# Performance work log

Hardware: AMD Instinct MI355X
Metric: run time of the kernel (lower is better)

Reference implementation:

```python
import jax, jax.numpy as jnp
import numpy as np

BS, H, W, A, NC, G = 2048, 14, 14, 5, 2, 30
SIZE = 1 + NC + 4  # conf, classes, x, y, w, h
OBJ_SCALE, NOOBJ_SCALE, CLASS_SCALE, COORD_SCALE = 5.0, 0.5, 1.0, 1.0


def setup_inputs() -> dict:
    key = jax.random.key(0)
    pred = jax.random.normal(key, (BS, A * SIZE, H, W), dtype=jnp.float32) * 0.5
    # Structured label: G ground-truth boxes per image at distinct cells.
    rng = np.random.default_rng(0)
    lab = np.zeros((BS, 7, H, W), np.float32)
    perm = np.argsort(rng.random((BS, H * W)), axis=1)[:, :G]  # distinct cells
    r, c = perm // W, perm % W
    b = np.arange(BS)[:, None]
    lab[b, 0, r, c] = 1.0
    cls = rng.integers(0, 2, (BS, G)).astype(np.float32)
    lab[b, 1, r, c] = cls
    lab[b, 2, r, c] = 1.0 - cls
    lab[b, 3, r, c] = rng.uniform(0.1, 0.9, (BS, G))  # tx in-cell offset
    lab[b, 4, r, c] = rng.uniform(0.1, 0.9, (BS, G))  # ty
    lab[b, 5, r, c] = rng.uniform(0.05, 0.4, (BS, G))  # tw (normalized)
    lab[b, 6, r, c] = rng.uniform(0.05, 0.4, (BS, G))  # th
    anchors = np.array([[42.0, 44.0], [91.0, 104.0], [162.0, 220.0],
                        [299.0, 170.0], [396.0, 359.0]], np.float32)
    return {"pred": pred, "label": jnp.asarray(lab),
            "anchors": jnp.asarray(anchors), "seen": 6400}


def _yolo_v2_loss(pred, label, anchors, seen):
    f32 = jnp.float32
    anchor_bias = anchors / (512.0 / 14.0) / jnp.array([W, H], f32)  # [A,2], grid-normalized
    # [BS,H,W,A,SIZE]
    pred_r = pred.transpose(0, 2, 3, 1).reshape(BS, H, W, A, SIZE)
    sxy = jax.nn.sigmoid(pred_r[..., 1 + NC:3 + NC])               # sigmoid(x,y)
    ids = jnp.stack(jnp.meshgrid(jnp.arange(W, dtype=f32),
                                 jnp.arange(H, dtype=f32)), -1)[:, :, None, :]  # [H,W,1,2]=(c,r)
    coords = (sxy + ids) / jnp.array([W, H], f32)                  # normalized centers
    wh = jnp.exp(pred_r[..., 3 + NC:5 + NC]) * anchor_bias         # normalized w,h
    boxes = jnp.concatenate([coords, wh], -1)                      # [BS,H,W,A,4]
    aw, ah = anchor_bias[:, 0], anchor_bias[:, 1]

    def per_image(pred_b, sxy_b, boxes_b, label_b):
        obj = label_b[0].reshape(-1)
        vals, flat = jax.lax.top_k(obj, G)
        valid = vals > 0                                           # [G]
        r = flat // W
        c = flat % W
        tx, ty = label_b[3, r, c], label_b[4, r, c]
        tw = jnp.where(valid, label_b[5, r, c], 1.0)
        th = jnp.where(valid, label_b[6, r, c], 1.0)
        # gt boxes are built from detached .data in the torch code -> stop_gradient
        gx = jax.lax.stop_gradient((tx + c.astype(f32)) / W)
        gy = jax.lax.stop_gradient((ty + r.astype(f32)) / H)
        tw = jax.lax.stop_gradient(tw)
        th = jax.lax.stop_gradient(th)
        # pairwise IoU pred boxes [H,W,A] vs gt [G] -> [H,W,A,G]
        x1, y1 = boxes_b[..., 0:1], boxes_b[..., 1:2]
        w1, h1 = boxes_b[..., 2:3], boxes_b[..., 3:4]
        xi1 = jnp.maximum(x1 - 0.5 * w1, gx - 0.5 * tw)
        yi1 = jnp.maximum(y1 - 0.5 * h1, gy - 0.5 * th)
        xi2 = jnp.minimum(x1 + 0.5 * w1, gx + 0.5 * tw)
        yi2 = jnp.minimum(y1 + 0.5 * h1, gy + 0.5 * th)
        inter = jnp.maximum(xi2 - xi1, 0.0) * jnp.maximum(yi2 - yi1, 0.0)
        union = w1 * h1 + tw * th - inter
        iou = jnp.maximum(inter / union, 0.0)
        iou = jnp.where(valid, iou, 0.0)
        noobj = (iou.max(-1) <= 0.6).astype(f32) * (NOOBJ_SCALE * pred_b[..., 0])
        if seen < 12800:
            prior = 0.01 * jnp.concatenate([sxy_b - 0.5,
                                            pred_b[..., 3 + NC:5 + NC]], -1)
        else:
            prior = jnp.zeros((H, W, A, 4), f32)
        coord_obj = jnp.concatenate([prior, noobj[..., None]], -1)  # [H,W,A,5]
        # best anchor per gt (IoU of (0,0,tw,th) vs (0,0,aw,ah))
        ia = jnp.minimum(tw[:, None], aw) * jnp.minimum(th[:, None], ah)
        aid = jnp.argmax(ia / (tw[:, None] * th[:, None] + aw * ah - ia), axis=1)
        wi = (gx * W).astype(jnp.int32)
        fx = gx * W - wi.astype(f32)
        hj = (gy * H).astype(jnp.int32)
        fy = gy * H - hj.astype(f32)
        twh = jnp.log(jnp.stack([tw, th], 1) / anchor_bias[aid])    # [G,2]
        truth_coords = jnp.concatenate([fx[:, None], fy[:, None], twh], 1)
        p_sel = pred_b[hj, wi, aid]                                 # [G,SIZE]
        pc = jnp.concatenate([sxy_b[hj, wi, aid], p_sel[:, 3 + NC:5 + NC]], 1)
        wgt = COORD_SCALE * (2.0 - fx * fy)                         # detached in torch
        closs = wgt[:, None] * (pc - truth_coords)                  # [G,4]
        iou_sel = iou[hj, wi, aid, jnp.arange(G)]                   # [G]
        objl = OBJ_SCALE * (p_sel[:, 0] - iou_sel)
        tco = jnp.concatenate([closs, objl[:, None]], 1) * valid[:, None].astype(f32)
        cvec = jnp.stack([label_b[1, hj, wi], label_b[2, hj, wi]], 1)
        cls_l = CLASS_SCALE * (p_sel[:, 1:1 + NC] - cvec)
        loss_cls = jnp.sum((cls_l ** 2) * valid[:, None].astype(f32))
        m = jnp.zeros((H, W, A), f32).at[hj, wi, aid].add(valid.astype(f32))
        ta = jnp.zeros((H, W, A, 5), f32).at[hj, wi, aid].add(tco)
        m4 = m[..., None]
        comb = m4 * ta + (1.0 - m4) * coord_obj
        il = loss_cls + jnp.sum(comb ** 2)
        return jnp.where(jnp.any(valid), il, 0.0)

    losses = jax.vmap(per_image)(pred_r, sxy, boxes, label)
    return jnp.reshape(jnp.sum(losses) / BS, (1,))


def reference(pred, label, anchors, seen):
    return _yolo_v2_loss(pred, label, anchors, seen)
```

## Files before the change

kernel.cpp:

```cpp
#include <hip/hip_runtime.h>
#include <math.h>

#define BS 2048
#define H_ 14
#define W_ 14
#define A_ 5
#define G_ 30
#define HW_ 196
#define NCELL 980
#define NTHREADS 256
#define LABN (7 * HW_)
#define LAB4 (LABN / 4)

__device__ __forceinline__ float fast_rcp(float x) { return __builtin_amdgcn_rcpf(x); }

__global__ __launch_bounds__(NTHREADS) void yolo_main(
    const float* __restrict__ pred,
    const float* __restrict__ label,
    const float* __restrict__ anchors,
    float* __restrict__ partial)
{
    __shared__ float  s_lab[LABN];
    __shared__ float4 s_box[G_];
    __shared__ float  s_thr[G_];
    __shared__ float  s_area[G_];
    __shared__ float4 s_tgt[G_];
    __shared__ float4 s_aux[G_];
    __shared__ float  s_aw[A_], s_ah[A_];
    __shared__ short  s_map[NCELL];
    __shared__ int    s_flat[G_];
    __shared__ int    s_wcnt[NTHREADS / 64];
    __shared__ float  s_red[NTHREADS / 64];

    const int b    = blockIdx.x;
    const int tid  = threadIdx.x;
    const int lane = tid & 63;
    const int wv   = tid >> 6;
    const float* lb = label + (size_t)b * LABN;
    const float* pb = pred  + (size_t)b * (A_ * 7 * HW_);

    float objv = (tid < HW_) ? lb[tid] : 0.0f;

    {
        const float4* l4 = (const float4*)lb;
        float4* s4 = (float4*)s_lab;
        for (int i = tid; i < LAB4; i += NTHREADS) s4[i] = l4[i];
    }
    for (int i = tid; i < NCELL; i += NTHREADS) s_map[i] = -1;
    if (tid < A_) {
        const float div1 = 512.0f / 14.0f;
        s_aw[tid] = anchors[2 * tid]     / div1 / (float)W_;
        s_ah[tid] = anchors[2 * tid + 1] / div1 / (float)H_;
    }

    unsigned long long bm = __ballot(objv > 0.0f);
    if (lane == 0) s_wcnt[wv] = __popcll(bm);
    __syncthreads();
    if (objv > 0.0f) {
        int rank = __popcll(bm & ((1ULL << lane) - 1ULL));
        for (int w2 = 0; w2 < wv; ++w2) rank += s_wcnt[w2];
        s_flat[rank] = tid;
    }
    __syncthreads();

    if (tid < G_) {
        int flat = s_flat[tid];
        int r = flat / W_, c = flat - r * W_;
        float tx = s_lab[3 * HW_ + flat];
        float ty = s_lab[4 * HW_ + flat];
        float tw = s_lab[5 * HW_ + flat];
        float th = s_lab[6 * HW_ + flat];
        float gx = (tx + (float)c) / (float)W_;
        float gy = (ty + (float)r) / (float)H_;
        int   wi = (int)(gx * (float)W_);
        int   hj = (int)(gy * (float)H_);
        float fx = gx * (float)W_ - (float)wi;
        float fy = gy * (float)H_ - (float)hj;
        float best = -1.0f; int aid = 0;
        for (int aa = 0; aa < A_; ++aa) {
            float ia = fminf(tw, s_aw[aa]) * fminf(th, s_ah[aa]);
            float m  = ia / (tw * th + s_aw[aa] * s_ah[aa] - ia);
            if (m > best) { best = m; aid = aa; }
        }
        s_box[tid]  = make_float4(gx - 0.5f * tw, gy - 0.5f * th,
                                  gx + 0.5f * tw, gy + 0.5f * th);
        s_area[tid] = tw * th;
        s_thr[tid]  = 0.375f * tw * th;
        s_tgt[tid]  = make_float4(fx, fy, __logf(tw / s_aw[aid]), __logf(th / s_ah[aid]));
        s_aux[tid]  = make_float4(2.0f - fx * fy,
                                  s_lab[1 * HW_ + hj * W_ + wi],
                                  s_lab[2 * HW_ + hj * W_ + wi],
                                  0.0f);
        s_map[(hj * W_ + wi) * A_ + aid] = (short)tid;
    }
    __syncthreads();

    float lsum = 0.0f;
    if (tid < 245) {
        int a   = tid / 49;
        int q   = tid - a * 49;
        int hw0 = 4 * q;
        const float4* p4 = (const float4*)(pb + a * 7 * HW_);
        float4 P0 = p4[0 * 49 + q];
        float4 P1 = p4[1 * 49 + q];
        float4 P2 = p4[2 * 49 + q];
        float4 P3 = p4[3 * 49 + q];
        float4 P4 = p4[4 * 49 + q];
        float4 P5 = p4[5 * 49 + q];
        float4 P6 = p4[6 * 49 + q];
        float p0v[4] = {P0.x, P0.y, P0.z, P0.w};
        float p1v[4] = {P1.x, P1.y, P1.z, P1.w};
        float p2v[4] = {P2.x, P2.y, P2.z, P2.w};
        float p3v[4] = {P3.x, P3.y, P3.z, P3.w};
        float p4v[4] = {P4.x, P4.y, P4.z, P4.w};
        float p5v[4] = {P5.x, P5.y, P5.z, P5.w};
        float p6v[4] = {P6.x, P6.y, P6.z, P6.w};

        float aw = s_aw[a], ah = s_ah[a];
        float sxv[4], syv[4], xlo[4], xhi[4], ylo[4], yhi[4], acc[4];
        #pragma unroll
        for (int j = 0; j < 4; ++j) {
            int hw = hw0 + j;
            int h  = hw / W_;
            int w  = hw - h * W_;
            float sx = fast_rcp(1.0f + __expf(-p3v[j]));
            float sy = fast_rcp(1.0f + __expf(-p4v[j]));
            float bw = __expf(p5v[j]) * aw;
            float bh = __expf(p6v[j]) * ah;
            float x1 = (sx + (float)w) * (1.0f / (float)W_);
            float y1 = (sy + (float)h) * (1.0f / (float)H_);
            sxv[j] = sx;  syv[j] = sy;
            xlo[j] = x1 - 0.5f * bw;  xhi[j] = x1 + 0.5f * bw;
            ylo[j] = y1 - 0.5f * bh;  yhi[j] = y1 + 0.5f * bh;
            acc[j] = -1e30f;
        }

        #pragma unroll 5
        for (int g = 0; g < G_; ++g) {
            float4 bx  = s_box[g];
            float  thr = s_thr[g];
            #pragma unroll
            for (int j = 0; j < 4; ++j) {
                float xi1 = fmaxf(xlo[j], bx.x);
                float yi1 = fmaxf(ylo[j], bx.y);
                float xi2 = fminf(xhi[j], bx.z);
                float yi2 = fminf(yhi[j], bx.w);
                float dx = fmaxf(xi2 - xi1, 0.0f);
                float dy = fmaxf(yi2 - yi1, 0.0f);
                acc[j] = fmaxf(acc[j], fmaf(dx, dy, -thr));
            }
        }

        #pragma unroll
        for (int j = 0; j < 4; ++j) {
            int g_at = s_map[(hw0 + j) * A_ + a];
            float area1 = (xhi[j] - xlo[j]) * (yhi[j] - ylo[j]);
            if (g_at >= 0) {
                float4 t  = s_tgt[g_at];
                float4 u  = s_aux[g_at];
                float4 bx = s_box[g_at];
                float xi1 = fmaxf(xlo[j], bx.x);
                float yi1 = fmaxf(ylo[j], bx.y);
                float xi2 = fminf(xhi[j], bx.z);
                float yi2 = fminf(yhi[j], bx.w);
                float inter = fmaxf(xi2 - xi1, 0.0f) * fmaxf(yi2 - yi1, 0.0f);
                float uni   = area1 + s_area[g_at] - inter;
                float iou   = fmaxf(inter * fast_rcp(uni), 0.0f);
                float wg = u.x;
                float d0 = wg * (sxv[j] - t.x);
                float d1 = wg * (syv[j] - t.y);
                float d2 = wg * (p5v[j] - t.z);
                float d3 = wg * (p6v[j] - t.w);
                float ob = 5.0f * (p0v[j] - iou);
                float c1 = p1v[j] - u.y;
                float c2 = p2v[j] - u.z;
                lsum += d0*d0 + d1*d1 + d2*d2 + d3*d3 + ob*ob + c1*c1 + c2*c2;
            } else {
                float pr0 = 0.01f * (sxv[j] - 0.5f);
                float pr1 = 0.01f * (syv[j] - 0.5f);
                float pr2 = 0.01f * p5v[j];
                float pr3 = 0.01f * p6v[j];
                float no  = (acc[j] <= 0.375f * area1) ? 0.5f * p0v[j] : 0.0f;
                lsum += pr0*pr0 + pr1*pr1 + pr2*pr2 + pr3*pr3 + no*no;
            }
        }
    }

    #pragma unroll
    for (int off = 32; off > 0; off >>= 1)
        lsum += __shfl_down(lsum, off, 64);
    if (lane == 0) s_red[wv] = lsum;
    __syncthreads();
    if (tid == 0) {
        float tot = 0.0f;
        #pragma unroll
        for (int i = 0; i < NTHREADS / 64; ++i) tot += s_red[i];
        partial[b] = tot;
    }
}

__global__ __launch_bounds__(NTHREADS) void yolo_reduce(
    const float* __restrict__ partial, float* __restrict__ out)
{
    __shared__ float s_red[NTHREADS / 64];
    const int tid = threadIdx.x, lane = tid & 63, wv = tid >> 6;
    float s = 0.0f;
    for (int i = tid; i < BS; i += NTHREADS) s += partial[i];
    #pragma unroll
    for (int off = 32; off > 0; off >>= 1)
        s += __shfl_down(s, off, 64);
    if (lane == 0) s_red[wv] = s;
    __syncthreads();
    if (tid == 0) {
        float tot = 0.0f;
        #pragma unroll
        for (int i = 0; i < NTHREADS / 64; ++i) tot += s_red[i];
        out[0] = tot * (1.0f / (float)BS);
    }
}

extern "C" void kernel_launch(void* const* d_in, const int* in_sizes, int n_in,
                              void* d_out, int out_size, void* d_ws, size_t ws_size,
                              hipStream_t stream) {
    const float* pred    = (const float*)d_in[0];
    const float* label   = (const float*)d_in[1];
    const float* anchors = (const float*)d_in[2];
    float* out     = (float*)d_out;
    float* partial = (float*)d_ws;

    yolo_main<<<dim3(BS), dim3(NTHREADS), 0, stream>>>(pred, label, anchors, partial);
    yolo_reduce<<<dim3(1), dim3(NTHREADS), 0, stream>>>(partial, out);
}
```

Before: 115.1 us.

## Split each image across two single-wave blocks with two work items per lane

Each image is now handled by two 64-thread blocks instead of one 256-thread block. Each lane processes two anchor/quad work items, and the block reduction is a single wave shuffle with no shared-memory stage. The label load, gt-box extraction and target setup are now done redundantly by both blocks of an image, which doubles label reads and setup work, in exchange for lighter per-block synchronization and more, smaller blocks. The cell-to-gt map shrinks from short to char, and the reduce kernel sums twice as many partials.

```diff
diff --git a/kernel.cpp b/kernel.cpp
--- a/kernel.cpp
+++ b/kernel.cpp
@@ -7,14 +7,15 @@
 #define A_ 5
 #define G_ 30
 #define HW_ 196
-#define NCELL 980
-#define NTHREADS 256
 #define LABN (7 * HW_)
 #define LAB4 (LABN / 4)
+#define NTH 64
+#define NQ 245
+#define NBLK (BS * 2)
 
 __device__ __forceinline__ float fast_rcp(float x) { return __builtin_amdgcn_rcpf(x); }
 
-__global__ __launch_bounds__(NTHREADS) void yolo_main(
+__global__ __launch_bounds__(NTH, 4) void yolo_main(
     const float* __restrict__ pred,
     const float* __restrict__ label,
     const float* __restrict__ anchors,
@@ -27,44 +28,51 @@
     __shared__ float4 s_tgt[G_];
     __shared__ float4 s_aux[G_];
     __shared__ float  s_aw[A_], s_ah[A_];
-    __shared__ short  s_map[NCELL];
     __shared__ int    s_flat[G_];
-    __shared__ int    s_wcnt[NTHREADS / 64];
-    __shared__ float  s_red[NTHREADS / 64];
-
-    const int b    = blockIdx.x;
-    const int tid  = threadIdx.x;
-    const int lane = tid & 63;
-    const int wv   = tid >> 6;
+    __shared__ char   s_map[992] __attribute__((aligned(16)));
+
+    const int blk  = blockIdx.x;
+    const int b    = blk >> 1;
+    const int half = blk & 1;
+    const int lane = threadIdx.x;
     const float* lb = label + (size_t)b * LABN;
     const float* pb = pred  + (size_t)b * (A_ * 7 * HW_);
 
-    float objv = (tid < HW_) ? lb[tid] : 0.0f;
-
     {
         const float4* l4 = (const float4*)lb;
         float4* s4 = (float4*)s_lab;
-        for (int i = tid; i < LAB4; i += NTHREADS) s4[i] = l4[i];
-    }
-    for (int i = tid; i < NCELL; i += NTHREADS) s_map[i] = -1;
-    if (tid < A_) {
+        #pragma unroll
+        for (int k = 0; k < 6; ++k) {
+            int i = k * NTH + lane;
+            if (i < LAB4) s4[i] = l4[i];
+        }
+    }
+    if (lane < 62) ((int4*)s_map)[lane] = make_int4(-1, -1, -1, -1);
+    if (lane < A_) {
         const float div1 = 512.0f / 14.0f;
-        s_aw[tid] = anchors[2 * tid]     / div1 / (float)W_;
-        s_ah[tid] = anchors[2 * tid + 1] / div1 / (float)H_;
-    }
-
-    unsigned long long bm = __ballot(objv > 0.0f);
-    if (lane == 0) s_wcnt[wv] = __popcll(bm);
-    __syncthreads();
-    if (objv > 0.0f) {
-        int rank = __popcll(bm & ((1ULL << lane) - 1ULL));
-        for (int w2 = 0; w2 < wv; ++w2) rank += s_wcnt[w2];
-        s_flat[rank] = tid;
-    }
-    __syncthreads();
-
-    if (tid < G_) {
-        int flat = s_flat[tid];
+        s_aw[lane] = anchors[2 * lane]     / div1 / (float)W_;
+        s_ah[lane] = anchors[2 * lane + 1] / div1 / (float)H_;
+    }
+    __syncthreads();
+
+    {
+        int base = 0;
+        #pragma unroll
+        for (int k = 0; k < 4; ++k) {
+            int idx = k * NTH + lane;
+            float v = (idx < HW_) ? s_lab[idx] : 0.0f;
+            unsigned long long m = __ballot(v > 0.0f);
+            if (v > 0.0f) {
+                int rank = base + __popcll(m & ((1ULL << lane) - 1ULL));
+                s_flat[rank] = idx;
+            }
+            base += __popcll(m);
+        }
+    }
+    __syncthreads();
+
+    if (lane < G_) {
+        int flat = s_flat[lane];
         int r = flat / W_, c = flat - r * W_;
         float tx = s_lab[3 * HW_ + flat];
         float ty = s_lab[4 * HW_ + flat];
@@ -82,39 +90,54 @@
             float m  = ia / (tw * th + s_aw[aa] * s_ah[aa] - ia);
             if (m > best) { best = m; aid = aa; }
         }
-        s_box[tid]  = make_float4(gx - 0.5f * tw, gy - 0.5f * th,
-                                  gx + 0.5f * tw, gy + 0.5f * th);
-        s_area[tid] = tw * th;
-        s_thr[tid]  = 0.375f * tw * th;
-        s_tgt[tid]  = make_float4(fx, fy, __logf(tw / s_aw[aid]), __logf(th / s_ah[aid]));
-        s_aux[tid]  = make_float4(2.0f - fx * fy,
-                                  s_lab[1 * HW_ + hj * W_ + wi],
-                                  s_lab[2 * HW_ + hj * W_ + wi],
-                                  0.0f);
-        s_map[(hj * W_ + wi) * A_ + aid] = (short)tid;
-    }
-    __syncthreads();
+        s_box[lane]  = make_float4(gx - 0.5f * tw, gy - 0.5f * th,
+                                   gx + 0.5f * tw, gy + 0.5f * th);
+        s_area[lane] = tw * th;
+        s_thr[lane]  = 0.375f * tw * th;
+        s_tgt[lane]  = make_float4(fx, fy, __logf(tw / s_aw[aid]), __logf(th / s_ah[aid]));
+        s_aux[lane]  = make_float4(2.0f - fx * fy,
+                                   s_lab[1 * HW_ + hj * W_ + wi],
+                                   s_lab[2 * HW_ + hj * W_ + wi],
+                                   0.0f);
+        s_map[(hj * W_ + wi) * A_ + aid] = (char)lane;
+    }
+    __syncthreads();
+
+    int  q0   = half * 128 + lane;
+    int  q1   = q0 + 64;
+    bool act1 = (q1 < NQ);
+    int  q1s  = act1 ? q1 : q0;
+
+    float4 P0[2], P1[2], P2[2], P3[2], P4[2], P5[2], P6[2];
+    {
+        int a0 = q0 / 49, qq = q0 - a0 * 49;
+        const float4* p4 = (const float4*)(pb + a0 * 7 * HW_);
+        P0[0]=p4[0*49+qq]; P1[0]=p4[1*49+qq]; P2[0]=p4[2*49+qq];
+        P3[0]=p4[3*49+qq]; P4[0]=p4[4*49+qq]; P5[0]=p4[5*49+qq]; P6[0]=p4[6*49+qq];
+    }
+    {
+        int a1 = q1s / 49, qq = q1s - a1 * 49;
+        const float4* p4 = (const float4*)(pb + a1 * 7 * HW_);
+        P0[1]=p4[0*49+qq]; P1[1]=p4[1*49+qq]; P2[1]=p4[2*49+qq];
+        P3[1]=p4[3*49+qq]; P4[1]=p4[4*49+qq]; P5[1]=p4[5*49+qq]; P6[1]=p4[6*49+qq];
+    }
 
     float lsum = 0.0f;
-    if (tid < 245) {
-        int a   = tid / 49;
-        int q   = tid - a * 49;
-        int hw0 = 4 * q;
-        const float4* p4 = (const float4*)(pb + a * 7 * HW_);
-        float4 P0 = p4[0 * 49 + q];
-        float4 P1 = p4[1 * 49 + q];
-        float4 P2 = p4[2 * 49 + q];
-        float4 P3 = p4[3 * 49 + q];
-        float4 P4 = p4[4 * 49 + q];
-        float4 P5 = p4[5 * 49 + q];
-        float4 P6 = p4[6 * 49 + q];
-        float p0v[4] = {P0.x, P0.y, P0.z, P0.w};
-        float p1v[4] = {P1.x, P1.y, P1.z, P1.w};
-        float p2v[4] = {P2.x, P2.y, P2.z, P2.w};
-        float p3v[4] = {P3.x, P3.y, P3.z, P3.w};
-        float p4v[4] = {P4.x, P4.y, P4.z, P4.w};
-        float p5v[4] = {P5.x, P5.y, P5.z, P5.w};
-        float p6v[4] = {P6.x, P6.y, P6.z, P6.w};
+    #pragma unroll
+    for (int t = 0; t < 2; ++t) {
+        bool act = (t == 0) | act1;
+        int  q   = t ? q1s : q0;
+        int  a   = q / 49;
+        int  qq  = q - a * 49;
+        int  hw0 = 4 * qq;
+
+        float p0v[4] = {P0[t].x, P0[t].y, P0[t].z, P0[t].w};
+        float p1v[4] = {P1[t].x, P1[t].y, P1[t].z, P1[t].w};
+        float p2v[4] = {P2[t].x, P2[t].y, P2[t].z, P2[t].w};
+        float p3v[4] = {P3[t].x, P3[t].y, P3[t].z, P3[t].w};
+        float p4v[4] = {P4[t].x, P4[t].y, P4[t].z, P4[t].w};
+        float p5v[4] = {P5[t].x, P5[t].y, P5[t].z, P5[t].w};
+        float p6v[4] = {P6[t].x, P6[t].y, P6[t].z, P6[t].w};
 
         float aw = s_aw[a], ah = s_ah[a];
         float sxv[4], syv[4], xlo[4], xhi[4], ylo[4], yhi[4], acc[4];
@@ -151,37 +174,39 @@
             }
         }
 
-        #pragma unroll
-        for (int j = 0; j < 4; ++j) {
-            int g_at = s_map[(hw0 + j) * A_ + a];
-            float area1 = (xhi[j] - xlo[j]) * (yhi[j] - ylo[j]);
-            if (g_at >= 0) {
-                float4 t  = s_tgt[g_at];
-                float4 u  = s_aux[g_at];
-                float4 bx = s_box[g_at];
-                float xi1 = fmaxf(xlo[j], bx.x);
-                float yi1 = fmaxf(ylo[j], bx.y);
-                float xi2 = fminf(xhi[j], bx.z);
-                float yi2 = fminf(yhi[j], bx.w);
-                float inter = fmaxf(xi2 - xi1, 0.0f) * fmaxf(yi2 - yi1, 0.0f);
-                float uni   = area1 + s_area[g_at] - inter;
-                float iou   = fmaxf(inter * fast_rcp(uni), 0.0f);
-                float wg = u.x;
-                float d0 = wg * (sxv[j] - t.x);
-                float d1 = wg * (syv[j] - t.y);
-                float d2 = wg * (p5v[j] - t.z);
-                float d3 = wg * (p6v[j] - t.w);
-                float ob = 5.0f * (p0v[j] - iou);
-                float c1 = p1v[j] - u.y;
-                float c2 = p2v[j] - u.z;
-                lsum += d0*d0 + d1*d1 + d2*d2 + d3*d3 + ob*ob + c1*c1 + c2*c2;
-            } else {
-                float pr0 = 0.01f * (sxv[j] - 0.5f);
-                float pr1 = 0.01f * (syv[j] - 0.5f);
-                float pr2 = 0.01f * p5v[j];
-                float pr3 = 0.01f * p6v[j];
-                float no  = (acc[j] <= 0.375f * area1) ? 0.5f * p0v[j] : 0.0f;
-                lsum += pr0*pr0 + pr1*pr1 + pr2*pr2 + pr3*pr3 + no*no;
+        if (act) {
+            #pragma unroll
+            for (int j = 0; j < 4; ++j) {
+                int g_at = (int)s_map[(hw0 + j) * A_ + a];
+                float area1 = (xhi[j] - xlo[j]) * (yhi[j] - ylo[j]);
+                if (g_at >= 0) {
+                    float4 tg = s_tgt[g_at];
+                    float4 u  = s_aux[g_at];
+                    float4 bx = s_box[g_at];
+                    float xi1 = fmaxf(xlo[j], bx.x);
+                    float yi1 = fmaxf(ylo[j], bx.y);
+                    float xi2 = fminf(xhi[j], bx.z);
+                    float yi2 = fminf(yhi[j], bx.w);
+                    float inter = fmaxf(xi2 - xi1, 0.0f) * fmaxf(yi2 - yi1, 0.0f);
+                    float uni   = area1 + s_area[g_at] - inter;
+                    float iou   = fmaxf(inter * fast_rcp(uni), 0.0f);
+                    float wg = u.x;
+                    float d0 = wg * (sxv[j] - tg.x);
+                    float d1 = wg * (syv[j] - tg.y);
+                    float d2 = wg * (p5v[j] - tg.z);
+                    float d3 = wg * (p6v[j] - tg.w);
+                    float ob = 5.0f * (p0v[j] - iou);
+                    float c1 = p1v[j] - u.y;
+                    float c2 = p2v[j] - u.z;
+                    lsum += d0*d0 + d1*d1 + d2*d2 + d3*d3 + ob*ob + c1*c1 + c2*c2;
+                } else {
+                    float pr0 = 0.01f * (sxv[j] - 0.5f);
+                    float pr1 = 0.01f * (syv[j] - 0.5f);
+                    float pr2 = 0.01f * p5v[j];
+                    float pr3 = 0.01f * p6v[j];
+                    float no  = (acc[j] <= 0.375f * area1) ? 0.5f * p0v[j] : 0.0f;
+                    lsum += pr0*pr0 + pr1*pr1 + pr2*pr2 + pr3*pr3 + no*no;
+                }
             }
         }
     }
@@ -189,23 +214,16 @@
     #pragma unroll
     for (int off = 32; off > 0; off >>= 1)
         lsum += __shfl_down(lsum, off, 64);
-    if (lane == 0) s_red[wv] = lsum;
-    __syncthreads();
-    if (tid == 0) {
-        float tot = 0.0f;
-        #pragma unroll
-        for (int i = 0; i < NTHREADS / 64; ++i) tot += s_red[i];
-        partial[b] = tot;
-    }
+    if (lane == 0) partial[blk] = lsum;
 }
 
-__global__ __launch_bounds__(NTHREADS) void yolo_reduce(
+__global__ __launch_bounds__(256) void yolo_reduce(
     const float* __restrict__ partial, float* __restrict__ out)
 {
-    __shared__ float s_red[NTHREADS / 64];
+    __shared__ float s_red[4];
     const int tid = threadIdx.x, lane = tid & 63, wv = tid >> 6;
     float s = 0.0f;
-    for (int i = tid; i < BS; i += NTHREADS) s += partial[i];
+    for (int i = tid; i < NBLK; i += 256) s += partial[i];
     #pragma unroll
     for (int off = 32; off > 0; off >>= 1)
         s += __shfl_down(s, off, 64);
@@ -214,7 +232,7 @@
     if (tid == 0) {
         float tot = 0.0f;
         #pragma unroll
-        for (int i = 0; i < NTHREADS / 64; ++i) tot += s_red[i];
+        for (int i = 0; i < 4; ++i) tot += s_red[i];
         out[0] = tot * (1.0f / (float)BS);
     }
 }
@@ -228,6 +246,6 @@
     float* out     = (float*)d_out;
     float* partial = (float*)d_ws;
 
-    yolo_main<<<dim3(BS), dim3(NTHREADS), 0, stream>>>(pred, label, anchors, partial);
-    yolo_reduce<<<dim3(1), dim3(NTHREADS), 0, stream>>>(partial, out);
+    yolo_main<<<dim3(NBLK), dim3(NTH), 0, stream>>>(pred, label, anchors, partial);
+    yolo_reduce<<<dim3(1), dim3(256), 0, stream>>>(partial, out);
 }
```

Result: slower. 118.1 us (+2.6%).

## Run IoU max-over-ground-truth loop in packed fp16 grid units

Applied to the files above, without the earlier changes.

Moves the per-cell max-IoU test against all ground-truth boxes into packed half-precision (two boxes per instruction), with box geometry kept in grid units so values fit fp16 range. The ground-truth geometry is packed into shared memory as h2 pairs, the map shrinks to char, and the class-channel prediction loads are deferred until after the loop to reduce register pressure. This halves the ALU work of the dominant loop but risks threshold misclassification near the 0.375 IoU boundary because of fp16 rounding.

```diff
diff --git a/kernel.cpp b/kernel.cpp
--- a/kernel.cpp
+++ b/kernel.cpp
@@ -7,12 +7,17 @@
 #define A_ 5
 #define G_ 30
 #define HW_ 196
-#define NCELL 980
 #define NTHREADS 256
 #define LABN (7 * HW_)
 #define LAB4 (LABN / 4)
+#define NQ 245
+
+typedef _Float16 h2 __attribute__((ext_vector_type(2)));
 
 __device__ __forceinline__ float fast_rcp(float x) { return __builtin_amdgcn_rcpf(x); }
+__device__ __forceinline__ h2 h2max(h2 a, h2 b) { return __builtin_elementwise_max(a, b); }
+__device__ __forceinline__ h2 h2min(h2 a, h2 b) { return __builtin_elementwise_min(a, b); }
+__device__ __forceinline__ h2 h2bc(float x) { h2 r; r[0] = (_Float16)x; r[1] = r[0]; return r; }
 
 __global__ __launch_bounds__(NTHREADS) void yolo_main(
     const float* __restrict__ pred,
@@ -21,13 +26,13 @@
     float* __restrict__ partial)
 {
     __shared__ float  s_lab[LABN];
-    __shared__ float4 s_box[G_];
-    __shared__ float  s_thr[G_];
-    __shared__ float  s_area[G_];
-    __shared__ float4 s_tgt[G_];
-    __shared__ float4 s_aux[G_];
+    __shared__ uint4  s_geo[16];
+    __shared__ unsigned int s_nth[16];
+    __shared__ float4 s_ebox[32];
+    __shared__ float4 s_tgt[32];
+    __shared__ float4 s_aux[32];
     __shared__ float  s_aw[A_], s_ah[A_];
-    __shared__ short  s_map[NCELL];
+    __shared__ char   s_map[992] __attribute__((aligned(16)));
     __shared__ int    s_flat[G_];
     __shared__ int    s_wcnt[NTHREADS / 64];
     __shared__ float  s_red[NTHREADS / 64];
@@ -46,11 +51,11 @@
         float4* s4 = (float4*)s_lab;
         for (int i = tid; i < LAB4; i += NTHREADS) s4[i] = l4[i];
     }
-    for (int i = tid; i < NCELL; i += NTHREADS) s_map[i] = -1;
+    if (tid < 62) ((int4*)s_map)[tid] = make_int4(-1, -1, -1, -1);
     if (tid < A_) {
         const float div1 = 512.0f / 14.0f;
-        s_aw[tid] = anchors[2 * tid]     / div1 / (float)W_;
-        s_ah[tid] = anchors[2 * tid + 1] / div1 / (float)H_;
+        s_aw[tid] = anchors[2 * tid]     / div1;
+        s_ah[tid] = anchors[2 * tid + 1] / div1;
     }
 
     unsigned long long bm = __ballot(objv > 0.0f);
@@ -70,54 +75,73 @@
         float ty = s_lab[4 * HW_ + flat];
         float tw = s_lab[5 * HW_ + flat];
         float th = s_lab[6 * HW_ + flat];
-        float gx = (tx + (float)c) / (float)W_;
-        float gy = (ty + (float)r) / (float)H_;
-        int   wi = (int)(gx * (float)W_);
-        int   hj = (int)(gy * (float)H_);
-        float fx = gx * (float)W_ - (float)wi;
-        float fy = gy * (float)H_ - (float)hj;
+        float gxg = tx + (float)c;
+        float gyg = ty + (float)r;
+        int   wi = (int)gxg;
+        int   hj = (int)gyg;
+        float fx = gxg - (float)wi;
+        float fy = gyg - (float)hj;
         float best = -1.0f; int aid = 0;
         for (int aa = 0; aa < A_; ++aa) {
-            float ia = fminf(tw, s_aw[aa]) * fminf(th, s_ah[aa]);
-            float m  = ia / (tw * th + s_aw[aa] * s_ah[aa] - ia);
+            float awn = s_aw[aa] / 14.0f;
+            float ahn = s_ah[aa] / 14.0f;
+            float ia = fminf(tw, awn) * fminf(th, ahn);
+            float m  = ia / (tw * th + awn * ahn - ia);
             if (m > best) { best = m; aid = aa; }
         }
-        s_box[tid]  = make_float4(gx - 0.5f * tw, gy - 0.5f * th,
-                                  gx + 0.5f * tw, gy + 0.5f * th);
-        s_area[tid] = tw * th;
-        s_thr[tid]  = 0.375f * tw * th;
-        s_tgt[tid]  = make_float4(fx, fy, __logf(tw / s_aw[aid]), __logf(th / s_ah[aid]));
+        float awn = s_aw[aid] / 14.0f, ahn = s_ah[aid] / 14.0f;
+        float twg = tw * 14.0f, thg = th * 14.0f;
+        float x1 = gxg - 0.5f * twg, y1 = gyg - 0.5f * thg;
+        float x2 = gxg + 0.5f * twg, y2 = gyg + 0.5f * thg;
+        float areag = twg * thg;
+        s_ebox[tid] = make_float4(x1, y1, x2, y2);
+        s_tgt[tid]  = make_float4(fx, fy, __logf(tw / awn), __logf(th / ahn));
         s_aux[tid]  = make_float4(2.0f - fx * fy,
                                   s_lab[1 * HW_ + hj * W_ + wi],
                                   s_lab[2 * HW_ + hj * W_ + wi],
-                                  0.0f);
-        s_map[(hj * W_ + wi) * A_ + aid] = (short)tid;
+                                  areag);
+        s_map[(hj * W_ + wi) * A_ + aid] = (char)tid;
+
+        _Float16* gp = (_Float16*)s_geo;
+        _Float16* np = (_Float16*)s_nth;
+        int p = tid >> 1, e = tid & 1;
+        gp[8 * p + 0 + e] = (_Float16)x1;
+        gp[8 * p + 2 + e] = (_Float16)y1;
+        gp[8 * p + 4 + e] = (_Float16)x2;
+        gp[8 * p + 6 + e] = (_Float16)y2;
+        np[2 * p + e]     = (_Float16)(-0.375f * areag);
+        if (tid < 2) {
+            int g2 = 30 + tid, p2 = g2 >> 1, e2 = g2 & 1;
+            gp[8 * p2 + 0 + e2] = (_Float16)x1;
+            gp[8 * p2 + 2 + e2] = (_Float16)y1;
+            gp[8 * p2 + 4 + e2] = (_Float16)x2;
+            gp[8 * p2 + 6 + e2] = (_Float16)y2;
+            np[2 * p2 + e2]     = (_Float16)(-0.375f * areag);
+        }
     }
     __syncthreads();
 
     float lsum = 0.0f;
-    if (tid < 245) {
+    if (tid < NQ) {
         int a   = tid / 49;
-        int q   = tid - a * 49;
-        int hw0 = 4 * q;
+        int qq  = tid - a * 49;
+        int hw0 = 4 * qq;
         const float4* p4 = (const float4*)(pb + a * 7 * HW_);
-        float4 P0 = p4[0 * 49 + q];
-        float4 P1 = p4[1 * 49 + q];
-        float4 P2 = p4[2 * 49 + q];
-        float4 P3 = p4[3 * 49 + q];
-        float4 P4 = p4[4 * 49 + q];
-        float4 P5 = p4[5 * 49 + q];
-        float4 P6 = p4[6 * 49 + q];
+        float4 P0 = p4[0 * 49 + qq];
+        float4 P3 = p4[3 * 49 + qq];
+        float4 P4 = p4[4 * 49 + qq];
+        float4 P5 = p4[5 * 49 + qq];
+        float4 P6 = p4[6 * 49 + qq];
         float p0v[4] = {P0.x, P0.y, P0.z, P0.w};
-        float p1v[4] = {P1.x, P1.y, P1.z, P1.w};
-        float p2v[4] = {P2.x, P2.y, P2.z, P2.w};
         float p3v[4] = {P3.x, P3.y, P3.z, P3.w};
         float p4v[4] = {P4.x, P4.y, P4.z, P4.w};
         float p5v[4] = {P5.x, P5.y, P5.z, P5.w};
         float p6v[4] = {P6.x, P6.y, P6.z, P6.w};
 
         float aw = s_aw[a], ah = s_ah[a];
-        float sxv[4], syv[4], xlo[4], xhi[4], ylo[4], yhi[4], acc[4];
+        float sxv[4], syv[4], bwv[4], bhv[4];
+        h2 xlo2[4], xhi2[4], ylo2[4], yhi2[4], acc2[4];
+        const h2 hz = h2bc(0.0f);
         #pragma unroll
         for (int j = 0; j < 4; ++j) {
             int hw = hw0 + j;
@@ -127,60 +151,78 @@
             float sy = fast_rcp(1.0f + __expf(-p4v[j]));
             float bw = __expf(p5v[j]) * aw;
             float bh = __expf(p6v[j]) * ah;
-            float x1 = (sx + (float)w) * (1.0f / (float)W_);
-            float y1 = (sy + (float)h) * (1.0f / (float)H_);
-            sxv[j] = sx;  syv[j] = sy;
-            xlo[j] = x1 - 0.5f * bw;  xhi[j] = x1 + 0.5f * bw;
-            ylo[j] = y1 - 0.5f * bh;  yhi[j] = y1 + 0.5f * bh;
-            acc[j] = -1e30f;
-        }
-
-        #pragma unroll 5
-        for (int g = 0; g < G_; ++g) {
-            float4 bx  = s_box[g];
-            float  thr = s_thr[g];
+            float x1 = sx + (float)w;
+            float y1 = sy + (float)h;
+            sxv[j] = sx;  syv[j] = sy;  bwv[j] = bw;  bhv[j] = bh;
+            xlo2[j] = h2bc(x1 - 0.5f * bw);
+            xhi2[j] = h2bc(x1 + 0.5f * bw);
+            ylo2[j] = h2bc(y1 - 0.5f * bh);
+            yhi2[j] = h2bc(y1 + 0.5f * bh);
+            acc2[j] = h2bc(-30000.0f);
+        }
+
+        #pragma unroll 4
+        for (int p = 0; p < 16; ++p) {
+            uint4 Gq = s_geo[p];
+            h2 X1 = __builtin_bit_cast(h2, Gq.x);
+            h2 Y1 = __builtin_bit_cast(h2, Gq.y);
+            h2 X2 = __builtin_bit_cast(h2, Gq.z);
+            h2 Y2 = __builtin_bit_cast(h2, Gq.w);
+            h2 NT = __builtin_bit_cast(h2, s_nth[p]);
             #pragma unroll
             for (int j = 0; j < 4; ++j) {
-                float xi1 = fmaxf(xlo[j], bx.x);
-                float yi1 = fmaxf(ylo[j], bx.y);
-                float xi2 = fminf(xhi[j], bx.z);
-                float yi2 = fminf(yhi[j], bx.w);
-                float dx = fmaxf(xi2 - xi1, 0.0f);
-                float dy = fmaxf(yi2 - yi1, 0.0f);
-                acc[j] = fmaxf(acc[j], fmaf(dx, dy, -thr));
+                h2 xi1 = h2max(xlo2[j], X1);
+                h2 yi1 = h2max(ylo2[j], Y1);
+                h2 xi2 = h2min(xhi2[j], X2);
+                h2 yi2 = h2min(yhi2[j], Y2);
+                h2 dx = h2max(xi2 - xi1, hz);
+                h2 dy = h2max(yi2 - yi1, hz);
+                acc2[j] = h2max(acc2[j], dx * dy + NT);
             }
         }
 
+        float4 R1 = p4[1 * 49 + qq];
+        float4 R2 = p4[2 * 49 + qq];
+        float p1v[4] = {R1.x, R1.y, R1.z, R1.w};
+        float p2v[4] = {R2.x, R2.y, R2.z, R2.w};
+
         #pragma unroll
         for (int j = 0; j < 4; ++j) {
-            int g_at = s_map[(hw0 + j) * A_ + a];
-            float area1 = (xhi[j] - xlo[j]) * (yhi[j] - ylo[j]);
+            int hw = hw0 + j;
+            int h  = hw / W_;
+            int w  = hw - h * W_;
+            int g_at = (int)s_map[hw * A_ + a];
+            float area1 = bwv[j] * bhv[j];
             if (g_at >= 0) {
-                float4 t  = s_tgt[g_at];
+                float4 tg = s_tgt[g_at];
                 float4 u  = s_aux[g_at];
-                float4 bx = s_box[g_at];
-                float xi1 = fmaxf(xlo[j], bx.x);
-                float yi1 = fmaxf(ylo[j], bx.y);
-                float xi2 = fminf(xhi[j], bx.z);
-                float yi2 = fminf(yhi[j], bx.w);
+                float4 bx = s_ebox[g_at];
+                float x1 = sxv[j] + (float)w, y1 = syv[j] + (float)h;
+                float xlo = x1 - 0.5f * bwv[j], xhi = x1 + 0.5f * bwv[j];
+                float ylo = y1 - 0.5f * bhv[j], yhi = y1 + 0.5f * bhv[j];
+                float xi1 = fmaxf(xlo, bx.x);
+                float yi1 = fmaxf(ylo, bx.y);
+                float xi2 = fminf(xhi, bx.z);
+                float yi2 = fminf(yhi, bx.w);
                 float inter = fmaxf(xi2 - xi1, 0.0f) * fmaxf(yi2 - yi1, 0.0f);
-                float uni   = area1 + s_area[g_at] - inter;
+                float uni   = area1 + u.w - inter;
                 float iou   = fmaxf(inter * fast_rcp(uni), 0.0f);
                 float wg = u.x;
-                float d0 = wg * (sxv[j] - t.x);
-                float d1 = wg * (syv[j] - t.y);
-                float d2 = wg * (p5v[j] - t.z);
-                float d3 = wg * (p6v[j] - t.w);
+                float d0 = wg * (sxv[j] - tg.x);
+                float d1 = wg * (syv[j] - tg.y);
+                float d2 = wg * (p5v[j] - tg.z);
+                float d3 = wg * (p6v[j] - tg.w);
                 float ob = 5.0f * (p0v[j] - iou);
                 float c1 = p1v[j] - u.y;
                 float c2 = p2v[j] - u.z;
                 lsum += d0*d0 + d1*d1 + d2*d2 + d3*d3 + ob*ob + c1*c1 + c2*c2;
             } else {
+                float accf = fmaxf((float)acc2[j][0], (float)acc2[j][1]);
                 float pr0 = 0.01f * (sxv[j] - 0.5f);
                 float pr1 = 0.01f * (syv[j] - 0.5f);
                 float pr2 = 0.01f * p5v[j];
                 float pr3 = 0.01f * p6v[j];
-                float no  = (acc[j] <= 0.375f * area1) ? 0.5f * p0v[j] : 0.0f;
+                float no  = (accf <= 0.375f * area1) ? 0.5f * p0v[j] : 0.0f;
                 lsum += pr0*pr0 + pr1*pr1 + pr2*pr2 + pr3*pr3 + no*no;
             }
         }
```

Measured after the change: 111.5 us, median of 2. 3.1% less time.
